# Kernel tuning notes

Measured on AMD Instinct MI355X. Metric: run time of the kernel, lower is better.

The kernel has to match this reference:

```python
import math
import jax, jax.numpy as jnp
import numpy as np

B, T, M, D = 65536, 20, 4, 4   # batch, timesteps, regions, d_reg
L, H, FF = 3, 2, 16            # layers, heads, dim_feedforward
S = M + 1                      # seq_len with cls token
TAU = 10000.0


def setup_inputs() -> dict:
    key = jax.random.key(0)
    ks = jax.random.split(key, 8)

    def w(k, shape, std=0.1):
        return jax.random.normal(k, shape, dtype=jnp.float32) * std

    return {
        "regional_states": jax.random.normal(ks[0], (B, T, M, D), dtype=jnp.float32),
        "cls_token": w(ks[1], (1, 1, D), 0.02),
        # stacked per-layer params (layer axis first)
        "Wqkv": w(ks[2], (L, 3 * D, D)),   # nn.MultiheadAttention in_proj_weight
        "bqkv": jnp.zeros((L, 3 * D), jnp.float32),
        "Wo": w(ks[3], (L, D, D)),          # out_proj weight
        "bo": jnp.zeros((L, D), jnp.float32),
        "W1": w(ks[4], (L, FF, D)),         # linear1 weight (torch layout: out, in)
        "b1": jnp.zeros((L, FF), jnp.float32),
        "W2": w(ks[5], (L, D, FF)),         # linear2 weight
        "b2": jnp.zeros((L, D), jnp.float32),
    }


def _positional_encoding():
    # PE(pos,2i)=sin(pos/tau^(2i/D)), PE(pos,2i+1)=cos(...)
    pos = jnp.arange(S, dtype=jnp.float32)[:, None]            # (S,1)
    div = jnp.exp(jnp.arange(0, D, 2, dtype=jnp.float32) * (-math.log(TAU) / D))
    pe = jnp.zeros((S, D), jnp.float32)
    pe = pe.at[:, 0::2].set(jnp.sin(pos * div))
    pe = pe.at[:, 1::2].set(jnp.cos(pos * div))
    return pe  # (S, D)


def _layer(x, Wqkv, bqkv, Wo, bo, W1, b1, W2, b2):
    # x: (N, S, D). Dropout is identity (eval mode).
    N, Sq, Dm = x.shape
    hd = Dm // H
    qkv = x @ Wqkv.T + bqkv                     # (N, S, 3D)
    q, k, v = jnp.split(qkv, 3, axis=-1)

    def heads(t):
        return t.reshape(N, Sq, H, hd).transpose(0, 2, 1, 3)  # (N, H, S, hd)

    q, k, v = heads(q), heads(k), heads(v)
    scores = jnp.einsum("nhqd,nhkd->nhqk", q, k) / math.sqrt(hd)
    attn = jax.nn.softmax(scores, axis=-1)
    o = jnp.einsum("nhqk,nhkd->nhqd", attn, v)
    o = o.transpose(0, 2, 1, 3).reshape(N, Sq, Dm)
    attn_out = o @ Wo.T + bo
    x = x + attn_out                            # residual (no norm)
    ff = jax.nn.relu(x @ W1.T + b1) @ W2.T + b2
    return x + ff


def reference(regional_states, cls_token, Wqkv, bqkv, Wo, bo, W1, b1, W2, b2):
    Bq, Tq, Mq, Dq = regional_states.shape
    N = Bq * Tq
    x = regional_states.reshape(N, Mq, Dq)
    cls = jnp.broadcast_to(cls_token, (N, 1, Dq))
    x = jnp.concatenate([cls, x], axis=1)       # (N, S, D)
    x = x + _positional_encoding()[None, :, :]
    for i in range(L):
        x = _layer(x, Wqkv[i], bqkv[i], Wo[i], bo[i], W1[i], b1[i], W2[i], b2[i])
    F_g = x[:, 0, :].reshape(Bq, Tq, Dq)
    subregion_seq = x[:, 1:, :].reshape(Bq, Tq, Mq * Dq)
    return (F_g, subregion_seq)
```

## Files before the change

### kernel.cpp

```cpp
#include <hip/hip_runtime.h>


typedef _Float16 h2 __attribute__((ext_vector_type(2)));

enum {
  WF_CLS  = 0,
  WF_BQKV = 4,
  WF_BO   = 40,
  WF_B2   = 52,
  H_B1    = 64,
  H_QKV   = 88,
  H_WO    = 160,
  H_W1    = 184,
  H_W2    = 280,
  WF_QKV0 = 376,
  WF_FLAG = 388,
  WF_TOTAL = 389
};

__device__ __forceinline__ float bf2f(unsigned short u) {
  unsigned int x = ((unsigned int)u) << 16;
  float f;
  __builtin_memcpy(&f, &x, 4);
  return f;
}

__device__ __forceinline__ bool is_bf16_packed(const unsigned int* w) {
  int pass = 0;
#pragma unroll
  for (int i = 0; i < 16; ++i) {
    unsigned int lo = w[i] & 0xFFFFu;
    unsigned int e = (lo >> 7) & 0xFFu;
    if (lo == 0u || (e >= 90u && e <= 140u)) ++pass;
  }
  return pass >= 15;
}

__device__ __forceinline__ float dot2(h2 a, h2 b, float c) {
#if __has_builtin(__builtin_amdgcn_fdot2)
  return __builtin_amdgcn_fdot2(a, b, c, false);
#else
  return fmaf((float)a.x, (float)b.x, fmaf((float)a.y, (float)b.y, c));
#endif
}

__device__ __forceinline__ h2 pk(float a, float b) {
  auto t = __builtin_amdgcn_cvt_pkrtz(a, b);
  h2 r;
  __builtin_memcpy(&r, &t, sizeof(r));
  return r;
}

__device__ __forceinline__ h2 relu2(h2 a) {
  h2 z = {(_Float16)0.0f, (_Float16)0.0f};
#if __has_builtin(__builtin_elementwise_max)
  return __builtin_elementwise_max(a, z);
#else
  h2 r;
  r.x = a.x > z.x ? a.x : z.x;
  r.y = a.y > z.y ? a.y : z.y;
  return r;
#endif
}

__device__ __forceinline__ float fexp2(float x) {
#if __has_builtin(__builtin_amdgcn_exp2f)
  return __builtin_amdgcn_exp2f(x);
#else
  return __builtin_exp2f(x);
#endif
}

__global__ void mpt_prep(const void* __restrict__ cls,
                         const void* __restrict__ Wqkv,
                         const void* __restrict__ bqkv,
                         const void* __restrict__ Wo,
                         const void* __restrict__ bo,
                         const void* __restrict__ W1,
                         const void* __restrict__ b1,
                         const void* __restrict__ W2,
                         const void* __restrict__ b2,
                         const void* __restrict__ xin,
                         float* __restrict__ wf) {
  const bool wbf = is_bf16_packed((const unsigned int*)Wqkv);
  const bool xbf = is_bf16_packed((const unsigned int*)xin);
  const float FS = 1.44269504088896341f * 0.70710678118654752f;

  for (int w = threadIdx.x; w < WF_TOTAL; w += 256) {
    if (w == WF_FLAG) { ((int*)wf)[w] = xbf ? 0 : 1; continue; }

    auto g = [&](const void* src, int idx) -> float {
      return wbf ? bf2f(((const unsigned short*)src)[idx])
                 : ((const float*)src)[idx];
    };

    if (w >= WF_QKV0) {
      int j = w - WF_QKV0;
      float acc = g(bqkv, j);
#pragma unroll
      for (int d = 0; d < 4; ++d) {
        float xc = g(cls, d) + ((d & 1) ? 1.0f : 0.0f);
        acc = fmaf(g(Wqkv, j * 4 + d), xc, acc);
      }
      if (j >= 4 && j < 8) acc *= FS;
      wf[w] = acc;
      continue;
    }

    if (w < H_B1) {
      float val;
      if (w < WF_BQKV) {
        val = g(cls, w) + ((w & 1) ? 1.0f : 0.0f);
      } else if (w < WF_BO) {
        int t = w - WF_BQKV;
        val = g(bqkv, t);
        int j = t % 12;
        if (j >= 4 && j < 8) val *= FS;
      } else if (w < WF_B2) {
        val = g(bo, w - WF_BO);
      } else {
        int t = w - WF_B2;
        val = g(b2, t) + g(bo, t);
      }
      wf[w] = val;
    } else {
      if (w < H_QKV) {
        int t = w - H_B1, l = t / 8, p = t % 8;
        int f0 = 2 * p, f1 = 2 * p + 1;
        float v0 = g(b1, l * 16 + f0), v1 = g(b1, l * 16 + f1);
#pragma unroll
        for (int d = 0; d < 4; ++d) {
          float bod = g(bo, l * 4 + d);
          v0 = fmaf(g(W1, l * 64 + f0 * 4 + d), bod, v0);
          v1 = fmaf(g(W1, l * 64 + f1 * 4 + d), bod, v1);
        }
        ((h2*)wf)[w] = pk(v0, v1);
      } else if (w < H_WO) {
        int t = w - H_QKV, l = t / 24, j = (t % 24) / 2, p = t & 1;
        int base = l * 48 + j * 4 + p * 2;
        float s = (j >= 4 && j < 8) ? FS : 1.0f;
        ((h2*)wf)[w] = pk(g(Wqkv, base) * s, g(Wqkv, base + 1) * s);
      } else if (w < H_W1) {
        int t = w - H_WO, l = t / 8, i = (t % 8) / 2, p = t & 1;
        int base = l * 16 + i * 4 + p * 2;
        ((h2*)wf)[w] = pk(g(Wo, base), g(Wo, base + 1));
      } else if (w < H_W2) {
        int t = w - H_W1, l = t / 32, p = (t % 32) / 4, d = t % 4;
        int base = l * 64 + 8 * p + d;
        ((h2*)wf)[w] = pk(g(W1, base), g(W1, base + 4));
      } else {
        int t = w - H_W2, l = t / 32, i = (t % 32) / 8, p = t % 8;
        int base = l * 64 + i * 16 + p * 2;
        ((h2*)wf)[w] = pk(g(W2, base), g(W2, base + 1));
      }
    }
  }
}

__global__ __launch_bounds__(256) void mpt_main(
    const void* __restrict__ xin,
    const float* __restrict__ wf,
    float* __restrict__ out,
    int N) {
  const int n = blockIdx.x * 256 + threadIdx.x;
  if (n >= N) return;

  const int xf32 = ((const int*)wf)[WF_FLAG];
  const h2* hw = (const h2*)wf;

  const float pe[4][4] = {
    { 0.8414709848078965f, 0.5403023058681398f, 0.0099998333341667f, 0.9999500004166653f },
    { 0.9092974268256817f,-0.4161468365471424f, 0.0199986666933331f, 0.9998000066665778f },
    { 0.1411200080598672f,-0.9899924966004454f, 0.0299955002024957f, 0.9995500337489875f },
    {-0.7568024953079283f,-0.6536436208636119f, 0.0399893341866342f, 0.9992001066609779f }
  };

  float raw[16];
  if (xf32) {
    const float4* pf = reinterpret_cast<const float4*>((const float*)xin + (size_t)n * 16);
#pragma unroll
    for (int r = 0; r < 4; ++r) {
      float4 t = pf[r];
      raw[r * 4 + 0] = t.x; raw[r * 4 + 1] = t.y;
      raw[r * 4 + 2] = t.z; raw[r * 4 + 3] = t.w;
    }
  } else {
    struct alignas(16) U8 { unsigned short v[8]; };
    const U8* p = reinterpret_cast<const U8*>((const unsigned short*)xin + (size_t)n * 16);
    U8 a0 = p[0], a1 = p[1];
#pragma unroll
    for (int j = 0; j < 8; ++j) {
      raw[j]     = bf2f(a0.v[j]);
      raw[8 + j] = bf2f(a1.v[j]);
    }
  }

  float x[5][4];
#pragma unroll
  for (int d = 0; d < 4; ++d) x[0][d] = wf[WF_CLS + d];
#pragma unroll
  for (int r = 0; r < 4; ++r)
#pragma unroll
    for (int d = 0; d < 4; ++d) x[1 + r][d] = raw[r * 4 + d] + pe[r][d];

  const h2 one2 = pk(1.0f, 1.0f);

#pragma unroll
  for (int l = 0; l < 3; ++l) {
    const float* bq  = wf + WF_BQKV + l * 12;
    const float* b2  = wf + WF_B2   + l * 4;
    const h2* hb1  = hw + H_B1  + l * 8;
    const h2* hq   = hw + H_QKV + l * 24;
    const h2* hwo  = hw + H_WO  + l * 8;
    const h2* hw1p = hw + H_W1  + l * 32;
    const h2* hw2  = hw + H_W2  + l * 32;

    h2 xh[5][2];
#pragma unroll
    for (int s = 0; s < 5; ++s) {
      if (l == 0 && s == 0) continue;
      xh[s][0] = pk(x[s][0], x[s][1]);
      xh[s][1] = pk(x[s][2], x[s][3]);
    }

    float q[5][4], k[5][4], v[5][4];
#pragma unroll
    for (int s = 0; s < 5; ++s) {
      if (l == 0 && s == 0) {
#pragma unroll
        for (int j = 0; j < 4; ++j) {
          q[0][j] = wf[WF_QKV0 + j];
          k[0][j] = wf[WF_QKV0 + 4 + j];
          v[0][j] = wf[WF_QKV0 + 8 + j];
        }
        continue;
      }
#pragma unroll
      for (int j = 0; j < 12; ++j) {
        float a = dot2(xh[s][0], hq[j * 2],
                       dot2(xh[s][1], hq[j * 2 + 1], bq[j]));
        if (j < 4)      q[s][j] = a;
        else if (j < 8) k[s][j - 4] = a;
        else            v[s][j - 8] = a;
      }
    }

    h2 oh[5][2];
#pragma unroll
    for (int h = 0; h < 2; ++h) {
      const int d0 = 2 * h, d1 = 2 * h + 1;
      h2 qh[5], kh[5];
#pragma unroll
      for (int s = 0; s < 5; ++s) {
        qh[s] = pk(q[s][d0], q[s][d1]);
        kh[s] = pk(k[s][d0], k[s][d1]);
      }
      h2 vp0[2], vp1[2];
      vp0[0] = pk(v[0][d0], v[1][d0]); vp0[1] = pk(v[2][d0], v[3][d0]);
      vp1[0] = pk(v[0][d1], v[1][d1]); vp1[1] = pk(v[2][d1], v[3][d1]);
#pragma unroll
      for (int si = 0; si < 5; ++si) {
        float e0 = fexp2(dot2(qh[si], kh[0], 0.0f));
        float e1 = fexp2(dot2(qh[si], kh[1], 0.0f));
        float e2 = fexp2(dot2(qh[si], kh[2], 0.0f));
        float e3 = fexp2(dot2(qh[si], kh[3], 0.0f));
        float e4 = fexp2(dot2(qh[si], kh[4], 0.0f));
        h2 ep0 = pk(e0, e1), ep1 = pk(e2, e3);
        float den = dot2(ep0, one2, dot2(ep1, one2, e4));
        float inv = __builtin_amdgcn_rcpf(den);
        float a0 = dot2(ep0, vp0[0], dot2(ep1, vp0[1], e4 * v[4][d0]));
        float a1 = dot2(ep0, vp1[0], dot2(ep1, vp1[1], e4 * v[4][d1]));
        oh[si][h] = pk(a0 * inv, a1 * inv);
      }
    }

#pragma unroll
    for (int s = 0; s < 5; ++s) {
      float nx[4];
#pragma unroll
      for (int i = 0; i < 4; ++i)
        nx[i] = dot2(oh[s][0], hwo[i * 2],
                     dot2(oh[s][1], hwo[i * 2 + 1], x[s][i]));

      h2 xb[4];
      float acc[4];
#pragma unroll
      for (int d = 0; d < 4; ++d) xb[d] = pk(nx[d], nx[d]);
#pragma unroll
      for (int i = 0; i < 4; ++i) acc[i] = b2[i];
#pragma unroll
      for (int p = 0; p < 8; ++p) {
        h2 hc = hb1[p];
#pragma unroll
        for (int d = 0; d < 4; ++d) hc = xb[d] * hw1p[p * 4 + d] + hc;
        h2 hh = relu2(hc);
#pragma unroll
        for (int i = 0; i < 4; ++i) acc[i] = dot2(hh, hw2[i * 8 + p], acc[i]);
      }
#pragma unroll
      for (int i = 0; i < 4; ++i) x[s][i] = nx[i] + acc[i];
    }
  }

  *reinterpret_cast<float4*>(out + (size_t)n * 4) =
      make_float4(x[0][0], x[0][1], x[0][2], x[0][3]);
  float* sub = out + (size_t)N * 4 + (size_t)n * 16;
#pragma unroll
  for (int r = 0; r < 4; ++r)
    *reinterpret_cast<float4*>(sub + r * 4) =
        make_float4(x[1 + r][0], x[1 + r][1], x[1 + r][2], x[1 + r][3]);
}

extern "C" void kernel_launch(void* const* d_in, const int* in_sizes, int n_in,
                              void* d_out, int out_size, void* d_ws, size_t ws_size,
                              hipStream_t stream) {
  float* wf = (float*)d_ws;

  mpt_prep<<<1, 256, 0, stream>>>(
      d_in[1], d_in[2], d_in[3], d_in[4], d_in[5],
      d_in[6], d_in[7], d_in[8], d_in[9],
      d_in[0],
      wf);

  const int N = in_sizes[0] / 16;
  mpt_main<<<(N + 255) / 256, 256, 0, stream>>>(
      d_in[0], wf, (float*)d_out, N);
}
```

Baseline: 254.3 us.

## Use persistent grid-stride loop with software-prefetch of next input row

The main kernel becomes a persistent grid-stride loop capped at 1280 blocks of 256 threads. Each thread loads the next sequence's input while it computes the current one, aiming to hide global load latency behind the ALU-heavy transformer math. The cost is higher register pressure from the prefetch buffers, which may lower occupancy. Fewer threads also means less latency hiding from wave switching, and the tail is less balanced.

```diff
diff --git a/kernel.cpp b/kernel.cpp
--- a/kernel.cpp
+++ b/kernel.cpp
@@ -162,8 +162,9 @@
     const float* __restrict__ wf,
     float* __restrict__ out,
     int N) {
-  const int n = blockIdx.x * 256 + threadIdx.x;
-  if (n >= N) return;
+  const int n0 = blockIdx.x * 256 + threadIdx.x;
+  if (n0 >= N) return;
+  const int stride = gridDim.x * 256;
 
   const int xf32 = ((const int*)wf)[WF_FLAG];
   const h2* hw = (const h2*)wf;
@@ -175,140 +176,173 @@
     {-0.7568024953079283f,-0.6536436208636119f, 0.0399893341866342f, 0.9992001066609779f }
   };
 
-  float raw[16];
+  const h2 one2 = pk(1.0f, 1.0f);
+
+  struct alignas(16) U8 { unsigned short v[8]; };
+  float4 pf[4];
+  U8 pb[2];
   if (xf32) {
-    const float4* pf = reinterpret_cast<const float4*>((const float*)xin + (size_t)n * 16);
-#pragma unroll
-    for (int r = 0; r < 4; ++r) {
-      float4 t = pf[r];
-      raw[r * 4 + 0] = t.x; raw[r * 4 + 1] = t.y;
-      raw[r * 4 + 2] = t.z; raw[r * 4 + 3] = t.w;
-    }
+    const float4* p = reinterpret_cast<const float4*>((const float*)xin + (size_t)n0 * 16);
+#pragma unroll
+    for (int r = 0; r < 4; ++r) pf[r] = p[r];
   } else {
-    struct alignas(16) U8 { unsigned short v[8]; };
-    const U8* p = reinterpret_cast<const U8*>((const unsigned short*)xin + (size_t)n * 16);
-    U8 a0 = p[0], a1 = p[1];
-#pragma unroll
-    for (int j = 0; j < 8; ++j) {
-      raw[j]     = bf2f(a0.v[j]);
-      raw[8 + j] = bf2f(a1.v[j]);
-    }
+    const U8* p = reinterpret_cast<const U8*>((const unsigned short*)xin + (size_t)n0 * 16);
+    pb[0] = p[0]; pb[1] = p[1];
   }
 
-  float x[5][4];
-#pragma unroll
-  for (int d = 0; d < 4; ++d) x[0][d] = wf[WF_CLS + d];
-#pragma unroll
-  for (int r = 0; r < 4; ++r)
-#pragma unroll
-    for (int d = 0; d < 4; ++d) x[1 + r][d] = raw[r * 4 + d] + pe[r][d];
-
-  const h2 one2 = pk(1.0f, 1.0f);
-
-#pragma unroll
-  for (int l = 0; l < 3; ++l) {
-    const float* bq  = wf + WF_BQKV + l * 12;
-    const float* b2  = wf + WF_B2   + l * 4;
-    const h2* hb1  = hw + H_B1  + l * 8;
-    const h2* hq   = hw + H_QKV + l * 24;
-    const h2* hwo  = hw + H_WO  + l * 8;
-    const h2* hw1p = hw + H_W1  + l * 32;
-    const h2* hw2  = hw + H_W2  + l * 32;
-
-    h2 xh[5][2];
-#pragma unroll
-    for (int s = 0; s < 5; ++s) {
-      if (l == 0 && s == 0) continue;
-      xh[s][0] = pk(x[s][0], x[s][1]);
-      xh[s][1] = pk(x[s][2], x[s][3]);
-    }
-
-    float q[5][4], k[5][4], v[5][4];
-#pragma unroll
-    for (int s = 0; s < 5; ++s) {
-      if (l == 0 && s == 0) {
-#pragma unroll
-        for (int j = 0; j < 4; ++j) {
-          q[0][j] = wf[WF_QKV0 + j];
-          k[0][j] = wf[WF_QKV0 + 4 + j];
-          v[0][j] = wf[WF_QKV0 + 8 + j];
-        }
-        continue;
-      }
-#pragma unroll
-      for (int j = 0; j < 12; ++j) {
-        float a = dot2(xh[s][0], hq[j * 2],
-                       dot2(xh[s][1], hq[j * 2 + 1], bq[j]));
-        if (j < 4)      q[s][j] = a;
-        else if (j < 8) k[s][j - 4] = a;
-        else            v[s][j - 8] = a;
-      }
-    }
-
-    h2 oh[5][2];
-#pragma unroll
-    for (int h = 0; h < 2; ++h) {
-      const int d0 = 2 * h, d1 = 2 * h + 1;
-      h2 qh[5], kh[5];
+#pragma unroll 1
+  for (int n = n0; n < N; n += stride) {
+    const int nn = n + stride;
+    float4 pfN[4];
+    U8 pbN[2];
+    if (nn < N) {
+      if (xf32) {
+        const float4* p = reinterpret_cast<const float4*>((const float*)xin + (size_t)nn * 16);
+#pragma unroll
+        for (int r = 0; r < 4; ++r) pfN[r] = p[r];
+      } else {
+        const U8* p = reinterpret_cast<const U8*>((const unsigned short*)xin + (size_t)nn * 16);
+        pbN[0] = p[0]; pbN[1] = p[1];
+      }
+    }
+
+    float raw[16];
+    if (xf32) {
+#pragma unroll
+      for (int r = 0; r < 4; ++r) {
+        raw[r * 4 + 0] = pf[r].x; raw[r * 4 + 1] = pf[r].y;
+        raw[r * 4 + 2] = pf[r].z; raw[r * 4 + 3] = pf[r].w;
+      }
+    } else {
+#pragma unroll
+      for (int j = 0; j < 8; ++j) {
+        raw[j]     = bf2f(pb[0].v[j]);
+        raw[8 + j] = bf2f(pb[1].v[j]);
+      }
+    }
+
+    float x[5][4];
+#pragma unroll
+    for (int d = 0; d < 4; ++d) x[0][d] = wf[WF_CLS + d];
+#pragma unroll
+    for (int r = 0; r < 4; ++r)
+#pragma unroll
+      for (int d = 0; d < 4; ++d) x[1 + r][d] = raw[r * 4 + d] + pe[r][d];
+
+#pragma unroll
+    for (int l = 0; l < 3; ++l) {
+      const float* bq  = wf + WF_BQKV + l * 12;
+      const float* b2  = wf + WF_B2   + l * 4;
+      const h2* hb1  = hw + H_B1  + l * 8;
+      const h2* hq   = hw + H_QKV + l * 24;
+      const h2* hwo  = hw + H_WO  + l * 8;
+      const h2* hw1p = hw + H_W1  + l * 32;
+      const h2* hw2  = hw + H_W2  + l * 32;
+
+      h2 xh[5][2];
 #pragma unroll
       for (int s = 0; s < 5; ++s) {
-        qh[s] = pk(q[s][d0], q[s][d1]);
-        kh[s] = pk(k[s][d0], k[s][d1]);
-      }
-      h2 vp0[2], vp1[2];
-      vp0[0] = pk(v[0][d0], v[1][d0]); vp0[1] = pk(v[2][d0], v[3][d0]);
-      vp1[0] = pk(v[0][d1], v[1][d1]); vp1[1] = pk(v[2][d1], v[3][d1]);
-#pragma unroll
-      for (int si = 0; si < 5; ++si) {
-        float e0 = fexp2(dot2(qh[si], kh[0], 0.0f));
-        float e1 = fexp2(dot2(qh[si], kh[1], 0.0f));
-        float e2 = fexp2(dot2(qh[si], kh[2], 0.0f));
-        float e3 = fexp2(dot2(qh[si], kh[3], 0.0f));
-        float e4 = fexp2(dot2(qh[si], kh[4], 0.0f));
-        h2 ep0 = pk(e0, e1), ep1 = pk(e2, e3);
-        float den = dot2(ep0, one2, dot2(ep1, one2, e4));
-        float inv = __builtin_amdgcn_rcpf(den);
-        float a0 = dot2(ep0, vp0[0], dot2(ep1, vp0[1], e4 * v[4][d0]));
-        float a1 = dot2(ep0, vp1[0], dot2(ep1, vp1[1], e4 * v[4][d1]));
-        oh[si][h] = pk(a0 * inv, a1 * inv);
-      }
-    }
-
-#pragma unroll
-    for (int s = 0; s < 5; ++s) {
-      float nx[4];
-#pragma unroll
-      for (int i = 0; i < 4; ++i)
-        nx[i] = dot2(oh[s][0], hwo[i * 2],
-                     dot2(oh[s][1], hwo[i * 2 + 1], x[s][i]));
-
-      h2 xb[4];
-      float acc[4];
-#pragma unroll
-      for (int d = 0; d < 4; ++d) xb[d] = pk(nx[d], nx[d]);
-#pragma unroll
-      for (int i = 0; i < 4; ++i) acc[i] = b2[i];
-#pragma unroll
-      for (int p = 0; p < 8; ++p) {
-        h2 hc = hb1[p];
-#pragma unroll
-        for (int d = 0; d < 4; ++d) hc = xb[d] * hw1p[p * 4 + d] + hc;
-        h2 hh = relu2(hc);
-#pragma unroll
-        for (int i = 0; i < 4; ++i) acc[i] = dot2(hh, hw2[i * 8 + p], acc[i]);
-      }
-#pragma unroll
-      for (int i = 0; i < 4; ++i) x[s][i] = nx[i] + acc[i];
+        if (l == 0 && s == 0) continue;
+        xh[s][0] = pk(x[s][0], x[s][1]);
+        xh[s][1] = pk(x[s][2], x[s][3]);
+      }
+
+      float q[5][4], k[5][4], v[5][4];
+#pragma unroll
+      for (int s = 0; s < 5; ++s) {
+        if (l == 0 && s == 0) {
+#pragma unroll
+          for (int j = 0; j < 4; ++j) {
+            q[0][j] = wf[WF_QKV0 + j];
+            k[0][j] = wf[WF_QKV0 + 4 + j];
+            v[0][j] = wf[WF_QKV0 + 8 + j];
+          }
+          continue;
+        }
+#pragma unroll
+        for (int j = 0; j < 12; ++j) {
+          float a = dot2(xh[s][0], hq[j * 2],
+                         dot2(xh[s][1], hq[j * 2 + 1], bq[j]));
+          if (j < 4)      q[s][j] = a;
+          else if (j < 8) k[s][j - 4] = a;
+          else            v[s][j - 8] = a;
+        }
+      }
+
+      h2 oh[5][2];
+#pragma unroll
+      for (int h = 0; h < 2; ++h) {
+        const int d0 = 2 * h, d1 = 2 * h + 1;
+        h2 qh[5], kh[5];
+#pragma unroll
+        for (int s = 0; s < 5; ++s) {
+          qh[s] = pk(q[s][d0], q[s][d1]);
+          kh[s] = pk(k[s][d0], k[s][d1]);
+        }
+        h2 vp0[2], vp1[2];
+        vp0[0] = pk(v[0][d0], v[1][d0]); vp0[1] = pk(v[2][d0], v[3][d0]);
+        vp1[0] = pk(v[0][d1], v[1][d1]); vp1[1] = pk(v[2][d1], v[3][d1]);
+#pragma unroll
+        for (int si = 0; si < 5; ++si) {
+          float e0 = fexp2(dot2(qh[si], kh[0], 0.0f));
+          float e1 = fexp2(dot2(qh[si], kh[1], 0.0f));
+          float e2 = fexp2(dot2(qh[si], kh[2], 0.0f));
+          float e3 = fexp2(dot2(qh[si], kh[3], 0.0f));
+          float e4 = fexp2(dot2(qh[si], kh[4], 0.0f));
+          h2 ep0 = pk(e0, e1), ep1 = pk(e2, e3);
+          float den = dot2(ep0, one2, dot2(ep1, one2, e4));
+          float inv = __builtin_amdgcn_rcpf(den);
+          float a0 = dot2(ep0, vp0[0], dot2(ep1, vp0[1], e4 * v[4][d0]));
+          float a1 = dot2(ep0, vp1[0], dot2(ep1, vp1[1], e4 * v[4][d1]));
+          oh[si][h] = pk(a0 * inv, a1 * inv);
+        }
+      }
+
+#pragma unroll
+      for (int s = 0; s < 5; ++s) {
+        float nx[4];
+#pragma unroll
+        for (int i = 0; i < 4; ++i)
+          nx[i] = dot2(oh[s][0], hwo[i * 2],
+                       dot2(oh[s][1], hwo[i * 2 + 1], x[s][i]));
+
+        h2 xb[4];
+        float acc[4];
+#pragma unroll
+        for (int d = 0; d < 4; ++d) xb[d] = pk(nx[d], nx[d]);
+#pragma unroll
+        for (int i = 0; i < 4; ++i) acc[i] = b2[i];
+#pragma unroll
+        for (int p = 0; p < 8; ++p) {
+          h2 hc = hb1[p];
+#pragma unroll
+          for (int d = 0; d < 4; ++d) hc = xb[d] * hw1p[p * 4 + d] + hc;
+          h2 hh = relu2(hc);
+#pragma unroll
+          for (int i = 0; i < 4; ++i) acc[i] = dot2(hh, hw2[i * 8 + p], acc[i]);
+        }
+#pragma unroll
+        for (int i = 0; i < 4; ++i) x[s][i] = nx[i] + acc[i];
+      }
+    }
+
+    *reinterpret_cast<float4*>(out + (size_t)n * 4) =
+        make_float4(x[0][0], x[0][1], x[0][2], x[0][3]);
+    float* sub = out + (size_t)N * 4 + (size_t)n * 16;
+#pragma unroll
+    for (int r = 0; r < 4; ++r)
+      *reinterpret_cast<float4*>(sub + r * 4) =
+          make_float4(x[1 + r][0], x[1 + r][1], x[1 + r][2], x[1 + r][3]);
+
+    if (nn < N) {
+      if (xf32) {
+#pragma unroll
+        for (int r = 0; r < 4; ++r) pf[r] = pfN[r];
+      } else {
+        pb[0] = pbN[0]; pb[1] = pbN[1];
+      }
     }
   }
-
-  *reinterpret_cast<float4*>(out + (size_t)n * 4) =
-      make_float4(x[0][0], x[0][1], x[0][2], x[0][3]);
-  float* sub = out + (size_t)N * 4 + (size_t)n * 16;
-#pragma unroll
-  for (int r = 0; r < 4; ++r)
-    *reinterpret_cast<float4*>(sub + r * 4) =
-        make_float4(x[1 + r][0], x[1 + r][1], x[1 + r][2], x[1 + r][3]);
 }
 
 extern "C" void kernel_launch(void* const* d_in, const int* in_sizes, int n_in,
@@ -323,6 +357,8 @@
       wf);
 
   const int N = in_sizes[0] / 16;
-  mpt_main<<<(N + 255) / 256, 256, 0, stream>>>(
+  int blocks = (N + 255) / 256;
+  if (blocks > 1280) blocks = 1280;
+  mpt_main<<<blocks, 256, 0, stream>>>(
       d_in[0], wf, (float*)d_out, N);
 }
```

Result: slower. 289.6 us (+13.9%).
